# Kernel tuning notes

Hardware: AMD Instinct MI355X
Metric: run time of the kernel (lower is better)

Reference implementation:

```python
import jax, jax.numpy as jnp
import numpy as np

EMB_DIM = 1024
NHEAD = 16
HEAD_DIM = EMB_DIM // NHEAD
SLEN = 1024
BSZ = 8
NEG_INF = -1e30


def setup_inputs() -> dict:
    key = jax.random.key(0)
    ks = jax.random.split(key, 8)
    q = jax.random.normal(ks[0], (SLEN, BSZ, EMB_DIM), dtype=jnp.float32)
    k = jax.random.normal(ks[1], (SLEN, BSZ, EMB_DIM), dtype=jnp.float32)
    v = jax.random.normal(ks[2], (SLEN, BSZ, EMB_DIM), dtype=jnp.float32)
    mask = jax.random.randint(ks[3], (BSZ * NHEAD, SLEN, SLEN), 0, 2).astype(jnp.bool_)
    # xavier_uniform bound for square [E,E] matrices
    bound = float(np.sqrt(6.0 / (EMB_DIM + EMB_DIM)))
    Wq = jax.random.uniform(ks[4], (EMB_DIM, EMB_DIM), jnp.float32, -bound, bound)
    Wk = jax.random.uniform(ks[5], (EMB_DIM, EMB_DIM), jnp.float32, -bound, bound)
    Wv = jax.random.uniform(ks[6], (EMB_DIM, EMB_DIM), jnp.float32, -bound, bound)
    Wo = jax.random.uniform(ks[7], (EMB_DIM, EMB_DIM), jnp.float32, -bound, bound)
    return {"q": q, "k": k, "v": v, "mask": mask, "Wq": Wq, "Wk": Wk, "Wv": Wv, "Wo": Wo}


def reference(q, k, v, mask, Wq, Wk, Wv, Wo):
    slen, bsz, emb = q.shape
    scaling = float(HEAD_DIM) ** -0.5
    # F.linear(x, W) = x @ W.T
    query = q @ Wq.T  # [slen, bsz, E]
    key_ = k @ Wk.T
    value = v @ Wv.T
    # -> [bsz*nhead, slen, head_dim]
    def split_heads(x):
        return x.reshape(slen, bsz * NHEAD, HEAD_DIM).transpose(1, 0, 2)
    query = split_heads(query)
    key_ = split_heads(key_)
    value = split_heads(value)
    attn_weight = jnp.einsum('bqd,bkd->bqk', query, key_) * scaling  # [B*H, S, S]
    attn_weight = jnp.where(mask, NEG_INF, attn_weight)
    attn_score = jax.nn.softmax(attn_weight, axis=-1)
    # attn_mask=True: post-softmax multiplicative mask
    attn_score = attn_score * (~mask).astype(attn_score.dtype)
    # dropout is identity in eval mode
    attn_output = jnp.einsum('bqk,bkd->bqd', attn_score, value)  # [B*H, S, hd]
    attn_output = attn_output.transpose(1, 0, 2).reshape(slen, bsz, emb)
    return attn_output @ Wo.T
```

## Files before the change

### kernel.cpp

```cpp
#include <hip/hip_runtime.h>


typedef __attribute__((ext_vector_type(8))) short bf16x8;
typedef __attribute__((ext_vector_type(8))) unsigned short u16x8;
typedef __attribute__((ext_vector_type(4))) float f32x4;

#define LOG2E 1.44269504088896340736f

__device__ __forceinline__ unsigned short bfbits(float f) {
  unsigned u = __builtin_bit_cast(unsigned, f);
  u += 0x7fffu + ((u >> 16) & 1u);
  return (unsigned short)(u >> 16);
}
__device__ __forceinline__ unsigned pk2(float a, float b) {
  return (unsigned)bfbits(a) | ((unsigned)bfbits(b) << 16);
}
__device__ __forceinline__ void async16(const void* src, void* dst_lds) {
  __builtin_amdgcn_global_load_lds(
      (const __attribute__((address_space(1))) unsigned int*)src,
      (__attribute__((address_space(3))) unsigned int*)dst_lds, 16, 0, 0);
}

__global__ __launch_bounds__(256) void cvt_kernel(
    const float* __restrict__ q, const float* __restrict__ k, const float* __restrict__ v,
    const float* __restrict__ wq, const float* __restrict__ wk,
    const float* __restrict__ wv, const float* __restrict__ wo,
    unsigned short* __restrict__ Xin, unsigned short* __restrict__ Wbf)
{
  const unsigned u = blockIdx.x * 256u + threadIdx.x;
  const float* src;
  unsigned short* dst;
  if (u < 3145728u) {
    const unsigned z = u >> 20, r = u & 1048575u;
    src = (z == 0 ? q : z == 1 ? k : v) + (size_t)r * 8;
    dst = Xin + (size_t)z * 8388608u + (size_t)r * 8;
  } else {
    const unsigned u2 = u - 3145728u, wz = u2 >> 17, r = u2 & 131071u;
    src = (wz == 0 ? wq : wz == 1 ? wk : wz == 2 ? wv : wo) + (size_t)r * 8;
    dst = Wbf + (size_t)wz * 1048576u + (size_t)r * 8;
  }
  f32x4 a = *(const f32x4*)src;
  f32x4 b = *(const f32x4*)(src + 4);
  u16x8 o;
  o[0]=bfbits(a[0]); o[1]=bfbits(a[1]); o[2]=bfbits(a[2]); o[3]=bfbits(a[3]);
  o[4]=bfbits(b[0]); o[5]=bfbits(b[1]); o[6]=bfbits(b[2]); o[7]=bfbits(b[3]);
  *(u16x8*)dst = o;
}

__global__ void detect_mask(const unsigned* __restrict__ m, int* __restrict__ flag)
{
  unsigned ok = 1u;
#pragma unroll 8
  for (int i = 0; i < 64; ++i) {
    unsigned w = m[(threadIdx.x << 6) + i];
    ok &= (w <= 1u) ? 1u : 0u;
  }
  unsigned long long vote = __ballot(ok != 0u);
  if (threadIdx.x == 0) *flag = (vote == ~0ull) ? 1 : 0;
}

template<int OUTF32>
__global__ __launch_bounds__(256) void gemm_bt(
    const unsigned short* __restrict__ A,
    const unsigned short* __restrict__ B,
    void* __restrict__ Cv, float scale, int M, int N, int K)
{
  const int tid = threadIdx.x;
  const int w = tid >> 6, lane = tid & 63, c = lane & 15, g = lane >> 4;
  const int wr = w >> 1, wc = w & 1;
  const int bx = blockIdx.x, by = blockIdx.y;
  __shared__ unsigned short As[128 * 32];
  __shared__ unsigned short Bs[128 * 32];
  f32x4 acc[4][4];
#pragma unroll
  for (int i = 0; i < 4; ++i)
#pragma unroll
    for (int j = 0; j < 4; ++j) acc[i][j] = (f32x4){0.f, 0.f, 0.f, 0.f};

  const int rowA = by * 128, rowB = bx * 128;
  const int sr = tid >> 2, sc = tid & 3;
  const int ldsbase = (tid & ~63) * 16;
  const int nk = K >> 5;
  for (int kt = 0; kt < nk; ++kt) {
    const int k0 = kt << 5;
#pragma unroll
    for (int i = 0; i < 2; ++i) {
      const int r = (i << 6) + sr;
      async16(A + (size_t)(rowA + r) * K + k0 + sc * 8, (char*)As + i * 4096 + ldsbase);
      async16(B + (size_t)(rowB + r) * K + k0 + sc * 8, (char*)Bs + i * 4096 + ldsbase);
    }
    __syncthreads();
    bf16x8 af[4], bfr[4];
#pragma unroll
    for (int mf = 0; mf < 4; ++mf)
      af[mf] = *(const bf16x8*)&As[(wr * 64 + mf * 16 + c) * 32 + g * 8];
#pragma unroll
    for (int nf = 0; nf < 4; ++nf)
      bfr[nf] = *(const bf16x8*)&Bs[(wc * 64 + nf * 16 + c) * 32 + g * 8];
#pragma unroll
    for (int mf = 0; mf < 4; ++mf)
#pragma unroll
      for (int nf = 0; nf < 4; ++nf)
        acc[mf][nf] = __builtin_amdgcn_mfma_f32_16x16x32_bf16(af[mf], bfr[nf], acc[mf][nf], 0, 0, 0);
    __syncthreads();
  }
  const int r0 = rowA + wr * 64, c0 = rowB + wc * 64;
  if (OUTF32) {
    float* O = (float*)Cv;
#pragma unroll
    for (int mf = 0; mf < 4; ++mf)
#pragma unroll
      for (int nf = 0; nf < 4; ++nf)
#pragma unroll
        for (int j = 0; j < 4; ++j)
          O[(size_t)(r0 + mf * 16 + g * 4 + j) * N + c0 + nf * 16 + c] = acc[mf][nf][j] * scale;
  } else {
    unsigned short* O = (unsigned short*)Cv;
#pragma unroll
    for (int mf = 0; mf < 4; ++mf)
#pragma unroll
      for (int nf = 0; nf < 4; ++nf)
#pragma unroll
        for (int j = 0; j < 4; ++j)
          O[(size_t)(r0 + mf * 16 + g * 4 + j) * N + c0 + nf * 16 + c] = bfbits(acc[mf][nf][j] * scale);
  }
}

__global__ __launch_bounds__(256) void transpose_v(
    const unsigned short* __restrict__ Xp2, unsigned short* __restrict__ Vt)
{
  const int tid = threadIdx.x;
  const int bh = blockIdx.y, b = bh >> 4, h = bh & 15;
  const int s0 = blockIdx.x << 6;
  __shared__ unsigned short T[64 * 68];
#pragma unroll
  for (int p = 0; p < 2; ++p) {
    const int idx = (p << 8) + tid, sr = idx >> 3, ch2 = idx & 7;
    *(u16x8*)&T[sr * 68 + ch2 * 8] =
        *(const u16x8*)(Xp2 + ((size_t)((s0 + sr) * 8 + b) << 10) + (h << 6) + ch2 * 8);
  }
  __syncthreads();
#pragma unroll
  for (int p = 0; p < 2; ++p) {
    const int idx = (p << 8) + tid, dr = idx >> 3, ch2 = idx & 7;
    u16x8 o;
#pragma unroll
    for (int e = 0; e < 8; ++e) o[e] = T[(ch2 * 8 + e) * 68 + dr];
    *(u16x8*)(Vt + ((size_t)(bh * 64 + dr) << 10) + s0 + ch2 * 8) = o;
  }
}

__global__ __launch_bounds__(256) void attn_kernel(
    const unsigned short* __restrict__ Qp,
    const unsigned short* __restrict__ Kp,
    const unsigned short* __restrict__ Vt,
    const void*           __restrict__ maskp,
    const int*            __restrict__ mflag,
    unsigned short* __restrict__ AO)
{
  const int tid = threadIdx.x;
  const int w = tid >> 6, lane = tid & 63, c = lane & 15, g = lane >> 4;
  const int bh = blockIdx.y, b = bh >> 4, h = bh & 15;
  const int qb0 = blockIdx.x << 6;
  const int qrow = qb0 + (w << 4) + c;
  const bool mi32 = (*mflag != 0);

  __shared__ unsigned short Ksm[64 * 72];
  __shared__ unsigned short Vsm[64 * 72];
  __shared__ unsigned short Psm[4][16 * 72];

  bf16x8 qf[2];
  {
    const unsigned short* qp = Qp + ((size_t)(qrow * 8 + b) << 10) + (h << 6) + (g << 3);
    qf[0] = *(const bf16x8*)qp;
    qf[1] = *(const bf16x8*)(qp + 32);
  }

  const int row0 = tid >> 3, ch = tid & 7;
  const unsigned short* Vg = Vt + ((size_t)bh << 16);

  bf16x8 kr[2], vr[2];
#pragma unroll
  for (int p = 0; p < 2; ++p) {
    const int r = row0 + p * 32;
    kr[p] = *(const bf16x8*)(Kp + ((size_t)(r * 8 + b) << 10) + (h << 6) + (ch << 3));
    vr[p] = *(const bf16x8*)(Vg + ((size_t)r << 10) + (ch << 3));
  }

  f32x4 oacc[4];
#pragma unroll
  for (int i = 0; i < 4; ++i) oacc[i] = (f32x4){0.f, 0.f, 0.f, 0.f};
  float mrun = -1e30f, lrun = 0.f;

  for (int t = 0; t < 16; ++t) {
    const int kk0 = t << 6;
    __syncthreads();
#pragma unroll
    for (int p = 0; p < 2; ++p) {
      const int r = row0 + p * 32;
      *(bf16x8*)&Ksm[r * 72 + (ch << 3)] = kr[p];
      *(bf16x8*)&Vsm[r * 72 + (ch << 3)] = vr[p];
    }
    __syncthreads();
    if (t < 15) {
      const int kk1 = kk0 + 64;
#pragma unroll
      for (int p = 0; p < 2; ++p) {
        const int r = row0 + p * 32;
        kr[p] = *(const bf16x8*)(Kp + ((size_t)((kk1 + r) * 8 + b) << 10) + (h << 6) + (ch << 3));
        vr[p] = *(const bf16x8*)(Vg + ((size_t)r << 10) + kk1 + (ch << 3));
      }
    }
    unsigned mv[4];
    if (mi32) {
      const int* mrow = (const int*)maskp + ((size_t)bh << 20) + ((size_t)qrow << 10) + kk0 + (g << 2);
#pragma unroll
      for (int mf = 0; mf < 4; ++mf) {
        const int4 w4 = *(const int4*)(mrow + mf * 16);
        mv[mf] = (w4.x ? 1u : 0u) | (w4.y ? 0x100u : 0u) | (w4.z ? 0x10000u : 0u) | (w4.w ? 0x1000000u : 0u);
      }
    } else {
      const unsigned char* mrow = (const unsigned char*)maskp + ((size_t)bh << 20) + ((size_t)qrow << 10) + kk0 + (g << 2);
#pragma unroll
      for (int mf = 0; mf < 4; ++mf) mv[mf] = *(const unsigned*)(mrow + mf * 16);
    }
    f32x4 sacc[4];
#pragma unroll
    for (int i = 0; i < 4; ++i) sacc[i] = (f32x4){0.f, 0.f, 0.f, 0.f};
#pragma unroll
    for (int d2 = 0; d2 < 2; ++d2) {
#pragma unroll
      for (int mf = 0; mf < 4; ++mf) {
        bf16x8 kf = *(const bf16x8*)&Ksm[(mf * 16 + c) * 72 + d2 * 32 + (g << 3)];
        sacc[mf] = __builtin_amdgcn_mfma_f32_16x16x32_bf16(kf, qf[d2], sacc[mf], 0, 0, 0);
      }
    }
    float tmax = -1e30f;
#pragma unroll
    for (int mf = 0; mf < 4; ++mf)
#pragma unroll
      for (int j = 0; j < 4; ++j) {
        float s = sacc[mf][j];
        if ((mv[mf] >> (8 * j)) & 0xffu) s = -1e30f;
        sacc[mf][j] = s;
        tmax = fmaxf(tmax, s);
      }
    tmax = fmaxf(tmax, __shfl_xor(tmax, 16));
    tmax = fmaxf(tmax, __shfl_xor(tmax, 32));
    const float mnew = fmaxf(mrun, tmax);
    const float alpha = __builtin_amdgcn_exp2f((mrun - mnew) * LOG2E);
    float tsum = 0.f;
    float pv[4][4];
#pragma unroll
    for (int mf = 0; mf < 4; ++mf)
#pragma unroll
      for (int j = 0; j < 4; ++j) {
        const float p = __builtin_amdgcn_exp2f((sacc[mf][j] - mnew) * LOG2E);
        pv[mf][j] = p;
        tsum += p;
      }
    tsum += __shfl_xor(tsum, 16);
    tsum += __shfl_xor(tsum, 32);
    lrun = lrun * alpha + tsum;
    mrun = mnew;
#pragma unroll
    for (int i = 0; i < 4; ++i) {
      oacc[i][0] *= alpha; oacc[i][1] *= alpha; oacc[i][2] *= alpha; oacc[i][3] *= alpha;
    }
#pragma unroll
    for (int mf = 0; mf < 4; ++mf) {
      uint2 t2;
      t2.x = pk2(pv[mf][0], pv[mf][1]);
      t2.y = pk2(pv[mf][2], pv[mf][3]);
      *(uint2*)&Psm[w][c * 72 + mf * 16 + (g << 2)] = t2;
    }
#pragma unroll
    for (int ks = 0; ks < 2; ++ks) {
      bf16x8 pf = *(const bf16x8*)&Psm[w][c * 72 + ks * 32 + (g << 3)];
#pragma unroll
      for (int mf = 0; mf < 4; ++mf) {
        bf16x8 vf = *(const bf16x8*)&Vsm[(mf * 16 + c) * 72 + ks * 32 + (g << 3)];
        oacc[mf] = __builtin_amdgcn_mfma_f32_16x16x32_bf16(vf, pf, oacc[mf], 0, 0, 0);
      }
    }
  }
  const float inv = 1.0f / lrun;
#pragma unroll
  for (int mf = 0; mf < 4; ++mf) {
    uint2 t2;
    t2.x = pk2(oacc[mf][0] * inv, oacc[mf][1] * inv);
    t2.y = pk2(oacc[mf][2] * inv, oacc[mf][3] * inv);
    *(uint2*)(AO + ((size_t)(qrow * 8 + b) << 10) + (h << 6) + mf * 16 + (g << 2)) = t2;
  }
}

extern "C" void kernel_launch(void* const* d_in, const int* in_sizes, int n_in,
                              void* d_out, int out_size, void* d_ws, size_t ws_size,
                              hipStream_t stream)
{
  const float* q  = (const float*)d_in[0];
  const float* k  = (const float*)d_in[1];
  const float* v  = (const float*)d_in[2];
  const void*  mask = (const void*)d_in[3];
  const float* wq = (const float*)d_in[4];
  const float* wk = (const float*)d_in[5];
  const float* wv = (const float*)d_in[6];
  const float* wo = (const float*)d_in[7];

  unsigned short* ws  = (unsigned short*)d_ws;
  unsigned short* Xin = ws;
  unsigned short* Wbf = ws + 25165824u;
  unsigned short* Xp  = ws + 29360128u;
  unsigned short* Vt  = ws + 8388608u;
  unsigned short* AO  = ws;
  int* mfl            = (int*)(ws + 16777216u);

  cvt_kernel<<<14336, 256, 0, stream>>>(q, k, v, wq, wk, wv, wo, Xin, Wbf);
  gemm_bt<0><<<dim3(8, 64), 256, 0, stream>>>(Xin,              Wbf,            Xp,              0.125f, 8192, 1024, 1024);
  gemm_bt<0><<<dim3(8, 64), 256, 0, stream>>>(Xin + 8388608u,   Wbf + 1048576u, Xp + 8388608u,   1.0f,   8192, 1024, 1024);
  gemm_bt<0><<<dim3(8, 64), 256, 0, stream>>>(Xin + 16777216u,  Wbf + 2097152u, Xp + 16777216u,  1.0f,   8192, 1024, 1024);
  detect_mask<<<1, 64, 0, stream>>>((const unsigned*)mask, mfl);
  transpose_v<<<dim3(16, 128), 256, 0, stream>>>(Xp + 16777216u, Vt);
  attn_kernel<<<dim3(16, 128), 256, 0, stream>>>(Xp, Xp + 8388608u, Vt, mask, mfl, AO);
  gemm_bt<1><<<dim3(8, 64), 256, 0, stream>>>(AO, Wbf + 3145728u, d_out, 1.0f, 8192, 1024, 1024);
}
```

Before: 346.2 us.

## Double-buffer GEMM tiles with 256x128 blocks, XCD swizzle, and prefetch attention mask

The projection GEMMs now use 512-thread blocks computing 256x128 tiles with a K-step of 64. Global-to-LDS async loads for the next K tile go into a second LDS buffer, which removes one barrier per step and overlaps loads with MFMA work. A block-index swizzle groups tiles for better L2 locality across XCDs. The attention kernel also issues the next tile's mask loads one iteration early to hide their latency, at the cost of more LDS per block (96KB) and more registers.

After: 311.6 us. -10.0%, faster.

```diff
diff --git a/kernel.cpp b/kernel.cpp
--- a/kernel.cpp
+++ b/kernel.cpp
@@ -60,7 +60,7 @@
 }
 
 template<int OUTF32>
-__global__ __launch_bounds__(256) void gemm_bt(
+__global__ __launch_bounds__(512) void gemm2ph(
     const unsigned short* __restrict__ A,
     const unsigned short* __restrict__ B,
     void* __restrict__ Cv, float scale, int M, int N, int K)
@@ -68,42 +68,68 @@
   const int tid = threadIdx.x;
   const int w = tid >> 6, lane = tid & 63, c = lane & 15, g = lane >> 4;
   const int wr = w >> 1, wc = w & 1;
-  const int bx = blockIdx.x, by = blockIdx.y;
-  __shared__ unsigned short As[128 * 32];
-  __shared__ unsigned short Bs[128 * 32];
+
+  const int nwg = gridDim.x, cpx = nwg >> 3, bid = blockIdx.x;
+  const int swz = (bid & 7) * cpx + (bid >> 3);
+  const int ntx = N >> 7;
+  const int bx = swz % ntx, by = swz / ntx;
+  const int rowA = by * 256, rowB = bx * 128;
+
+  __shared__ unsigned short As[2][256 * 64];
+  __shared__ unsigned short Bs[2][128 * 64];
+
   f32x4 acc[4][4];
 #pragma unroll
   for (int i = 0; i < 4; ++i)
 #pragma unroll
     for (int j = 0; j < 4; ++j) acc[i][j] = (f32x4){0.f, 0.f, 0.f, 0.f};
 
-  const int rowA = by * 128, rowB = bx * 128;
-  const int sr = tid >> 2, sc = tid & 3;
-  const int ldsbase = (tid & ~63) * 16;
-  const int nk = K >> 5;
+  const int srow = tid >> 3, skc = tid & 7;
+  const int wbase = (tid & ~63) * 16;
+
+#pragma unroll
+  for (int i = 0; i < 4; ++i)
+    async16(A + (size_t)(rowA + i * 64 + srow) * K + skc * 8,
+            (char*)&As[0][0] + i * 8192 + wbase);
+#pragma unroll
+  for (int j = 0; j < 2; ++j)
+    async16(B + (size_t)(rowB + j * 64 + srow) * K + skc * 8,
+            (char*)&Bs[0][0] + j * 8192 + wbase);
+  __syncthreads();
+
+  int buf = 0;
+  const int nk = K >> 6;
   for (int kt = 0; kt < nk; ++kt) {
-    const int k0 = kt << 5;
-#pragma unroll
-    for (int i = 0; i < 2; ++i) {
-      const int r = (i << 6) + sr;
-      async16(A + (size_t)(rowA + r) * K + k0 + sc * 8, (char*)As + i * 4096 + ldsbase);
-      async16(B + (size_t)(rowB + r) * K + k0 + sc * 8, (char*)Bs + i * 4096 + ldsbase);
-    }
+    if (kt + 1 < nk) {
+      const int k1 = (kt + 1) << 6, bo = buf ^ 1;
+#pragma unroll
+      for (int i = 0; i < 4; ++i)
+        async16(A + (size_t)(rowA + i * 64 + srow) * K + k1 + skc * 8,
+                (char*)&As[bo][0] + i * 8192 + wbase);
+#pragma unroll
+      for (int j = 0; j < 2; ++j)
+        async16(B + (size_t)(rowB + j * 64 + srow) * K + k1 + skc * 8,
+                (char*)&Bs[bo][0] + j * 8192 + wbase);
+    }
+    bf16x8 af[4][2], bfr[4][2];
+#pragma unroll
+    for (int x = 0; x < 4; ++x)
+#pragma unroll
+      for (int ks = 0; ks < 2; ++ks) {
+        af[x][ks]  = *(const bf16x8*)&As[buf][(wr * 64 + x * 16 + c) * 64 + ks * 32 + (g << 3)];
+        bfr[x][ks] = *(const bf16x8*)&Bs[buf][(wc * 64 + x * 16 + c) * 64 + ks * 32 + (g << 3)];
+      }
+#pragma unroll
+    for (int ks = 0; ks < 2; ++ks)
+#pragma unroll
+      for (int mf = 0; mf < 4; ++mf)
+#pragma unroll
+        for (int nf = 0; nf < 4; ++nf)
+          acc[mf][nf] = __builtin_amdgcn_mfma_f32_16x16x32_bf16(af[mf][ks], bfr[nf][ks], acc[mf][nf], 0, 0, 0);
     __syncthreads();
-    bf16x8 af[4], bfr[4];
-#pragma unroll
-    for (int mf = 0; mf < 4; ++mf)
-      af[mf] = *(const bf16x8*)&As[(wr * 64 + mf * 16 + c) * 32 + g * 8];
-#pragma unroll
-    for (int nf = 0; nf < 4; ++nf)
-      bfr[nf] = *(const bf16x8*)&Bs[(wc * 64 + nf * 16 + c) * 32 + g * 8];
-#pragma unroll
-    for (int mf = 0; mf < 4; ++mf)
-#pragma unroll
-      for (int nf = 0; nf < 4; ++nf)
-        acc[mf][nf] = __builtin_amdgcn_mfma_f32_16x16x32_bf16(af[mf], bfr[nf], acc[mf][nf], 0, 0, 0);
-    __syncthreads();
-  }
+    buf ^= 1;
+  }
+
   const int r0 = rowA + wr * 64, c0 = rowB + wc * 64;
   if (OUTF32) {
     float* O = (float*)Cv;
@@ -147,6 +173,22 @@
 #pragma unroll
     for (int e = 0; e < 8; ++e) o[e] = T[(ch2 * 8 + e) * 68 + dr];
     *(u16x8*)(Vt + ((size_t)(bh * 64 + dr) << 10) + s0 + ch2 * 8) = o;
+  }
+}
+
+__device__ __forceinline__ void load_mask4(unsigned mv[4], const void* maskp, bool mi32,
+                                           size_t base, int g) {
+  if (mi32) {
+    const int* mrow = (const int*)maskp + base + (g << 2);
+#pragma unroll
+    for (int mf = 0; mf < 4; ++mf) {
+      const int4 w4 = *(const int4*)(mrow + mf * 16);
+      mv[mf] = (w4.x ? 1u : 0u) | (w4.y ? 0x100u : 0u) | (w4.z ? 0x10000u : 0u) | (w4.w ? 0x1000000u : 0u);
+    }
+  } else {
+    const unsigned char* mrow = (const unsigned char*)maskp + base + (g << 2);
+#pragma unroll
+    for (int mf = 0; mf < 4; ++mf) mv[mf] = *(const unsigned*)(mrow + mf * 16);
   }
 }
 
@@ -178,6 +220,7 @@
 
   const int row0 = tid >> 3, ch = tid & 7;
   const unsigned short* Vg = Vt + ((size_t)bh << 16);
+  const size_t mbase0 = ((size_t)bh << 20) + ((size_t)qrow << 10);
 
   bf16x8 kr[2], vr[2];
 #pragma unroll
@@ -186,6 +229,8 @@
     kr[p] = *(const bf16x8*)(Kp + ((size_t)(r * 8 + b) << 10) + (h << 6) + (ch << 3));
     vr[p] = *(const bf16x8*)(Vg + ((size_t)r << 10) + (ch << 3));
   }
+  unsigned mv[4];
+  load_mask4(mv, maskp, mi32, mbase0, g);
 
   f32x4 oacc[4];
 #pragma unroll
@@ -202,6 +247,7 @@
       *(bf16x8*)&Vsm[r * 72 + (ch << 3)] = vr[p];
     }
     __syncthreads();
+    unsigned mvN[4];
     if (t < 15) {
       const int kk1 = kk0 + 64;
 #pragma unroll
@@ -210,19 +256,7 @@
         kr[p] = *(const bf16x8*)(Kp + ((size_t)((kk1 + r) * 8 + b) << 10) + (h << 6) + (ch << 3));
         vr[p] = *(const bf16x8*)(Vg + ((size_t)r << 10) + kk1 + (ch << 3));
       }
-    }
-    unsigned mv[4];
-    if (mi32) {
-      const int* mrow = (const int*)maskp + ((size_t)bh << 20) + ((size_t)qrow << 10) + kk0 + (g << 2);
-#pragma unroll
-      for (int mf = 0; mf < 4; ++mf) {
-        const int4 w4 = *(const int4*)(mrow + mf * 16);
-        mv[mf] = (w4.x ? 1u : 0u) | (w4.y ? 0x100u : 0u) | (w4.z ? 0x10000u : 0u) | (w4.w ? 0x1000000u : 0u);
-      }
-    } else {
-      const unsigned char* mrow = (const unsigned char*)maskp + ((size_t)bh << 20) + ((size_t)qrow << 10) + kk0 + (g << 2);
-#pragma unroll
-      for (int mf = 0; mf < 4; ++mf) mv[mf] = *(const unsigned*)(mrow + mf * 16);
+      load_mask4(mvN, maskp, mi32, mbase0 + kk1, g);
     }
     f32x4 sacc[4];
 #pragma unroll
@@ -282,6 +316,9 @@
         bf16x8 vf = *(const bf16x8*)&Vsm[(mf * 16 + c) * 72 + ks * 32 + (g << 3)];
         oacc[mf] = __builtin_amdgcn_mfma_f32_16x16x32_bf16(vf, pf, oacc[mf], 0, 0, 0);
       }
+    }
+    if (t < 15) {
+      mv[0] = mvN[0]; mv[1] = mvN[1]; mv[2] = mvN[2]; mv[3] = mvN[3];
     }
   }
   const float inv = 1.0f / lrun;
@@ -316,11 +353,11 @@
   int* mfl            = (int*)(ws + 16777216u);
 
   cvt_kernel<<<14336, 256, 0, stream>>>(q, k, v, wq, wk, wv, wo, Xin, Wbf);
-  gemm_bt<0><<<dim3(8, 64), 256, 0, stream>>>(Xin,              Wbf,            Xp,              0.125f, 8192, 1024, 1024);
-  gemm_bt<0><<<dim3(8, 64), 256, 0, stream>>>(Xin + 8388608u,   Wbf + 1048576u, Xp + 8388608u,   1.0f,   8192, 1024, 1024);
-  gemm_bt<0><<<dim3(8, 64), 256, 0, stream>>>(Xin + 16777216u,  Wbf + 2097152u, Xp + 16777216u,  1.0f,   8192, 1024, 1024);
+  gemm2ph<0><<<256, 512, 0, stream>>>(Xin,             Wbf,            Xp,             0.125f, 8192, 1024, 1024);
+  gemm2ph<0><<<256, 512, 0, stream>>>(Xin + 8388608u,  Wbf + 1048576u, Xp + 8388608u,  1.0f,   8192, 1024, 1024);
+  gemm2ph<0><<<256, 512, 0, stream>>>(Xin + 16777216u, Wbf + 2097152u, Xp + 16777216u, 1.0f,   8192, 1024, 1024);
   detect_mask<<<1, 64, 0, stream>>>((const unsigned*)mask, mfl);
   transpose_v<<<dim3(16, 128), 256, 0, stream>>>(Xp + 16777216u, Vt);
   attn_kernel<<<dim3(16, 128), 256, 0, stream>>>(Xp, Xp + 8388608u, Vt, mask, mfl, AO);
-  gemm_bt<1><<<dim3(8, 64), 256, 0, stream>>>(AO, Wbf + 3145728u, d_out, 1.0f, 8192, 1024, 1024);
-}
+  gemm2ph<1><<<256, 512, 0, stream>>>(AO, Wbf + 3145728u, d_out, 1.0f, 8192, 1024, 1024);
+}
```

## Pre-pack mask to bits inside projection GEMMs and double-buffer larger GEMM tiles

Applied to the files above, without the earlier changes.

The boolean mask is packed into 64-bit words by extra blocks appended to the three projection GEMM launches, so the attention kernel reads one bit per element instead of one byte or int. The GEMM becomes 256x128 tiles with 512 threads, double-buffered LDS loads and a swizzled block order. The aim is to cut mask bandwidth in attention and hide GEMM load latency, in exchange for extra workspace and a more complex GEMM launch.

New measurement: 343.5 us. About the same (-0.8%).

```diff
diff --git a/kernel.cpp b/kernel.cpp
--- a/kernel.cpp
+++ b/kernel.cpp
@@ -19,6 +19,18 @@
   __builtin_amdgcn_global_load_lds(
       (const __attribute__((address_space(1))) unsigned int*)src,
       (__attribute__((address_space(3))) unsigned int*)dst_lds, 16, 0, 0);
+}
+
+__global__ void detect_mask(const unsigned* __restrict__ m, int* __restrict__ flag)
+{
+  unsigned ok = 1u;
+#pragma unroll 8
+  for (int i = 0; i < 64; ++i) {
+    unsigned w = m[(threadIdx.x << 6) + i];
+    ok &= (w <= 1u) ? 1u : 0u;
+  }
+  unsigned long long vote = __ballot(ok != 0u);
+  if (threadIdx.x == 0) *flag = (vote == ~0ull) ? 1 : 0;
 }
 
 __global__ __launch_bounds__(256) void cvt_kernel(
@@ -41,69 +53,108 @@
   }
   f32x4 a = *(const f32x4*)src;
   f32x4 b = *(const f32x4*)(src + 4);
-  u16x8 o;
-  o[0]=bfbits(a[0]); o[1]=bfbits(a[1]); o[2]=bfbits(a[2]); o[3]=bfbits(a[3]);
-  o[4]=bfbits(b[0]); o[5]=bfbits(b[1]); o[6]=bfbits(b[2]); o[7]=bfbits(b[3]);
-  *(u16x8*)dst = o;
-}
-
-__global__ void detect_mask(const unsigned* __restrict__ m, int* __restrict__ flag)
-{
-  unsigned ok = 1u;
-#pragma unroll 8
-  for (int i = 0; i < 64; ++i) {
-    unsigned w = m[(threadIdx.x << 6) + i];
-    ok &= (w <= 1u) ? 1u : 0u;
-  }
-  unsigned long long vote = __ballot(ok != 0u);
-  if (threadIdx.x == 0) *flag = (vote == ~0ull) ? 1 : 0;
+  uint4 o;
+  o.x = pk2(a[0], a[1]); o.y = pk2(a[2], a[3]);
+  o.z = pk2(b[0], b[1]); o.w = pk2(b[2], b[3]);
+  *(uint4*)dst = o;
 }
 
 template<int OUTF32>
-__global__ __launch_bounds__(256) void gemm_bt(
+__global__ __launch_bounds__(512) void gemm2ph(
     const unsigned short* __restrict__ A,
     const unsigned short* __restrict__ B,
-    void* __restrict__ Cv, float scale, int M, int N, int K)
+    void* __restrict__ Cv, float scale, int M, int N, int K,
+    const void* __restrict__ maskp, const int* __restrict__ mflag,
+    unsigned long long* __restrict__ Mp, unsigned packLo, unsigned packHi)
 {
   const int tid = threadIdx.x;
+  __shared__ unsigned short As[2][256 * 32];
+  __shared__ unsigned short Bs[2][128 * 32];
+
+  if (blockIdx.x >= 256u) {
+    const unsigned u = packLo + (blockIdx.x - 256u) * 512u + tid;
+    if (u < packHi) {
+      unsigned long long bits = 0ull;
+      if (*mflag) {
+        const int4* src = (const int4*)((const int*)maskp + (size_t)u * 64);
+#pragma unroll
+        for (int i = 0; i < 16; ++i) {
+          const int4 w4 = src[i];
+          const unsigned nib = (w4.x ? 1u : 0u) | (w4.y ? 2u : 0u) |
+                               (w4.z ? 4u : 0u) | (w4.w ? 8u : 0u);
+          bits |= (unsigned long long)nib << (i * 4);
+        }
+      } else {
+        const uint4* src = (const uint4*)((const unsigned char*)maskp + (size_t)u * 64);
+#pragma unroll
+        for (int i = 0; i < 4; ++i) {
+          const uint4 w4 = src[i];
+          unsigned lo = 0;
+#pragma unroll
+          for (int b2 = 0; b2 < 4; ++b2) {
+            lo |= ((w4.x >> (8 * b2)) & 0xFFu) ? (1u << b2)        : 0u;
+            lo |= ((w4.y >> (8 * b2)) & 0xFFu) ? (1u << (4 + b2))  : 0u;
+            lo |= ((w4.z >> (8 * b2)) & 0xFFu) ? (1u << (8 + b2))  : 0u;
+            lo |= ((w4.w >> (8 * b2)) & 0xFFu) ? (1u << (12 + b2)) : 0u;
+          }
+          bits |= (unsigned long long)lo << (i * 16);
+        }
+      }
+      Mp[u] = bits;
+    }
+    return;
+  }
+
   const int w = tid >> 6, lane = tid & 63, c = lane & 15, g = lane >> 4;
   const int wr = w >> 1, wc = w & 1;
-  const int bx = blockIdx.x, by = blockIdx.y;
-  __shared__ unsigned short As[128 * 32];
-  __shared__ unsigned short Bs[128 * 32];
+  const int bid = blockIdx.x;
+  const int swz = (bid & 7) * 32 + (bid >> 3);
+  const int ntx = N >> 7;
+  const int bx = swz % ntx, by = swz / ntx;
+  const int rowA = by * 256, rowB = bx * 128;
+
   f32x4 acc[4][4];
 #pragma unroll
   for (int i = 0; i < 4; ++i)
 #pragma unroll
     for (int j = 0; j < 4; ++j) acc[i][j] = (f32x4){0.f, 0.f, 0.f, 0.f};
 
-  const int rowA = by * 128, rowB = bx * 128;
-  const int sr = tid >> 2, sc = tid & 3;
-  const int ldsbase = (tid & ~63) * 16;
+  const int srow = tid >> 2, skc = tid & 3;
+  const int wbase = (tid & ~63) * 16;
+
+#pragma unroll
+  for (int i = 0; i < 2; ++i)
+    async16(A + (size_t)(rowA + i * 128 + srow) * K + skc * 8,
+            (char*)&As[0][0] + i * 8192 + wbase);
+  async16(B + (size_t)(rowB + srow) * K + skc * 8, (char*)&Bs[0][0] + wbase);
+  __syncthreads();
+
+  int buf = 0;
   const int nk = K >> 5;
   for (int kt = 0; kt < nk; ++kt) {
-    const int k0 = kt << 5;
-#pragma unroll
-    for (int i = 0; i < 2; ++i) {
-      const int r = (i << 6) + sr;
-      async16(A + (size_t)(rowA + r) * K + k0 + sc * 8, (char*)As + i * 4096 + ldsbase);
-      async16(B + (size_t)(rowB + r) * K + k0 + sc * 8, (char*)Bs + i * 4096 + ldsbase);
-    }
-    __syncthreads();
+    if (kt + 1 < nk) {
+      const int k1 = (kt + 1) << 5, bo = buf ^ 1;
+#pragma unroll
+      for (int i = 0; i < 2; ++i)
+        async16(A + (size_t)(rowA + i * 128 + srow) * K + k1 + skc * 8,
+                (char*)&As[bo][0] + i * 8192 + wbase);
+      async16(B + (size_t)(rowB + srow) * K + k1 + skc * 8, (char*)&Bs[bo][0] + wbase);
+    }
     bf16x8 af[4], bfr[4];
 #pragma unroll
-    for (int mf = 0; mf < 4; ++mf)
-      af[mf] = *(const bf16x8*)&As[(wr * 64 + mf * 16 + c) * 32 + g * 8];
-#pragma unroll
-    for (int nf = 0; nf < 4; ++nf)
-      bfr[nf] = *(const bf16x8*)&Bs[(wc * 64 + nf * 16 + c) * 32 + g * 8];
+    for (int x = 0; x < 4; ++x) {
+      af[x]  = *(const bf16x8*)&As[buf][(wr * 64 + x * 16 + c) * 32 + (g << 3)];
+      bfr[x] = *(const bf16x8*)&Bs[buf][(wc * 64 + x * 16 + c) * 32 + (g << 3)];
+    }
 #pragma unroll
     for (int mf = 0; mf < 4; ++mf)
 #pragma unroll
       for (int nf = 0; nf < 4; ++nf)
         acc[mf][nf] = __builtin_amdgcn_mfma_f32_16x16x32_bf16(af[mf], bfr[nf], acc[mf][nf], 0, 0, 0);
     __syncthreads();
-  }
+    buf ^= 1;
+  }
+
   const int r0 = rowA + wr * 64, c0 = rowB + wc * 64;
   if (OUTF32) {
     float* O = (float*)Cv;
@@ -154,8 +205,7 @@
     const unsigned short* __restrict__ Qp,
     const unsigned short* __restrict__ Kp,
     const unsigned short* __restrict__ Vt,
-    const void*           __restrict__ maskp,
-    const int*            __restrict__ mflag,
+    const unsigned long long* __restrict__ Mp,
     unsigned short* __restrict__ AO)
 {
   const int tid = threadIdx.x;
@@ -163,7 +213,6 @@
   const int bh = blockIdx.y, b = bh >> 4, h = bh & 15;
   const int qb0 = blockIdx.x << 6;
   const int qrow = qb0 + (w << 4) + c;
-  const bool mi32 = (*mflag != 0);
 
   __shared__ unsigned short Ksm[64 * 72];
   __shared__ unsigned short Vsm[64 * 72];
@@ -178,6 +227,7 @@
 
   const int row0 = tid >> 3, ch = tid & 7;
   const unsigned short* Vg = Vt + ((size_t)bh << 16);
+  const unsigned long long* Mrow = Mp + (((size_t)bh << 10) + qrow) * 16;
 
   bf16x8 kr[2], vr[2];
 #pragma unroll
@@ -186,6 +236,7 @@
     kr[p] = *(const bf16x8*)(Kp + ((size_t)(r * 8 + b) << 10) + (h << 6) + (ch << 3));
     vr[p] = *(const bf16x8*)(Vg + ((size_t)r << 10) + (ch << 3));
   }
+  unsigned long long mw = Mrow[0];
 
   f32x4 oacc[4];
 #pragma unroll
@@ -202,6 +253,7 @@
       *(bf16x8*)&Vsm[r * 72 + (ch << 3)] = vr[p];
     }
     __syncthreads();
+    unsigned long long mwN = 0ull;
     if (t < 15) {
       const int kk1 = kk0 + 64;
 #pragma unroll
@@ -210,19 +262,7 @@
         kr[p] = *(const bf16x8*)(Kp + ((size_t)((kk1 + r) * 8 + b) << 10) + (h << 6) + (ch << 3));
         vr[p] = *(const bf16x8*)(Vg + ((size_t)r << 10) + kk1 + (ch << 3));
       }
-    }
-    unsigned mv[4];
-    if (mi32) {
-      const int* mrow = (const int*)maskp + ((size_t)bh << 20) + ((size_t)qrow << 10) + kk0 + (g << 2);
-#pragma unroll
-      for (int mf = 0; mf < 4; ++mf) {
-        const int4 w4 = *(const int4*)(mrow + mf * 16);
-        mv[mf] = (w4.x ? 1u : 0u) | (w4.y ? 0x100u : 0u) | (w4.z ? 0x10000u : 0u) | (w4.w ? 0x1000000u : 0u);
-      }
-    } else {
-      const unsigned char* mrow = (const unsigned char*)maskp + ((size_t)bh << 20) + ((size_t)qrow << 10) + kk0 + (g << 2);
-#pragma unroll
-      for (int mf = 0; mf < 4; ++mf) mv[mf] = *(const unsigned*)(mrow + mf * 16);
+      mwN = Mrow[t + 1];
     }
     f32x4 sacc[4];
 #pragma unroll
@@ -237,14 +277,16 @@
     }
     float tmax = -1e30f;
 #pragma unroll
-    for (int mf = 0; mf < 4; ++mf)
+    for (int mf = 0; mf < 4; ++mf) {
+      const unsigned nib = ((unsigned)(mw >> (mf * 16 + (g << 2)))) & 0xFu;
 #pragma unroll
       for (int j = 0; j < 4; ++j) {
         float s = sacc[mf][j];
-        if ((mv[mf] >> (8 * j)) & 0xffu) s = -1e30f;
+        if ((nib >> j) & 1u) s = -1e30f;
         sacc[mf][j] = s;
         tmax = fmaxf(tmax, s);
       }
+    }
     tmax = fmaxf(tmax, __shfl_xor(tmax, 16));
     tmax = fmaxf(tmax, __shfl_xor(tmax, 32));
     const float mnew = fmaxf(mrun, tmax);
@@ -283,6 +325,7 @@
         oacc[mf] = __builtin_amdgcn_mfma_f32_16x16x32_bf16(vf, pf, oacc[mf], 0, 0, 0);
       }
     }
+    mw = mwN;
   }
   const float inv = 1.0f / lrun;
 #pragma unroll
@@ -311,16 +354,25 @@
   unsigned short* Xin = ws;
   unsigned short* Wbf = ws + 25165824u;
   unsigned short* Xp  = ws + 29360128u;
+  unsigned long long* Mp = (unsigned long long*)(ws + 54525952u);
+  int* mfl            = (int*)(ws + 62914560u);
   unsigned short* Vt  = ws + 8388608u;
   unsigned short* AO  = ws;
-  int* mfl            = (int*)(ws + 16777216u);
-
+
+  const unsigned PT = 2097152u;
+  const unsigned p1 = 699051u, p2 = 1398102u;
+  const int packGrid = 256 + 1366;
+
+  detect_mask<<<1, 64, 0, stream>>>((const unsigned*)mask, mfl);
   cvt_kernel<<<14336, 256, 0, stream>>>(q, k, v, wq, wk, wv, wo, Xin, Wbf);
-  gemm_bt<0><<<dim3(8, 64), 256, 0, stream>>>(Xin,              Wbf,            Xp,              0.125f, 8192, 1024, 1024);
-  gemm_bt<0><<<dim3(8, 64), 256, 0, stream>>>(Xin + 8388608u,   Wbf + 1048576u, Xp + 8388608u,   1.0f,   8192, 1024, 1024);
-  gemm_bt<0><<<dim3(8, 64), 256, 0, stream>>>(Xin + 16777216u,  Wbf + 2097152u, Xp + 16777216u,  1.0f,   8192, 1024, 1024);
-  detect_mask<<<1, 64, 0, stream>>>((const unsigned*)mask, mfl);
+  gemm2ph<0><<<packGrid, 512, 0, stream>>>(Xin,             Wbf,            Xp,             0.125f, 8192, 1024, 1024,
+                                           mask, mfl, Mp, 0u, p1);
+  gemm2ph<0><<<packGrid, 512, 0, stream>>>(Xin + 8388608u,  Wbf + 1048576u, Xp + 8388608u,  1.0f,   8192, 1024, 1024,
+                                           mask, mfl, Mp, p1, p2);
+  gemm2ph<0><<<packGrid, 512, 0, stream>>>(Xin + 16777216u, Wbf + 2097152u, Xp + 16777216u, 1.0f,   8192, 1024, 1024,
+                                           mask, mfl, Mp, p2, PT);
   transpose_v<<<dim3(16, 128), 256, 0, stream>>>(Xp + 16777216u, Vt);
-  attn_kernel<<<dim3(16, 128), 256, 0, stream>>>(Xp, Xp + 8388608u, Vt, mask, mfl, AO);
-  gemm_bt<1><<<dim3(8, 64), 256, 0, stream>>>(AO, Wbf + 3145728u, d_out, 1.0f, 8192, 1024, 1024);
-}
+  attn_kernel<<<dim3(16, 128), 256, 0, stream>>>(Xp, Xp + 8388608u, Vt, Mp, AO);
+  gemm2ph<1><<<256, 512, 0, stream>>>(AO, Wbf + 3145728u, d_out, 1.0f, 8192, 1024, 1024,
+                                      mask, mfl, Mp, 0u, 0u);
+}
```
